# Optimization experiments

Measured on AMD Instinct MI355X. Metric: run time of the kernel, lower is better.

The kernel has to match this reference:

```python
import jax, jax.numpy as jnp
import numpy as np

NEG_SLOPE = 0.2
EPS = 1e-12


def setup_inputs() -> dict:
    key = jax.random.key(0)
    k1, k2, k3, k4, k5 = jax.random.split(key, 5)
    N, E, IN, OUT = 100000, 1600000, 256, 64
    x = jax.random.normal(k1, (N, IN), dtype=jnp.float32)
    edge_index = jax.random.randint(k2, (2, E), 0, N, dtype=jnp.int64)
    # GATConv (heads=1) parameters: lin weight, att_src, att_dst, bias
    W = jax.random.normal(k3, (IN, OUT), dtype=jnp.float32) * (1.0 / np.sqrt(IN))
    att_src = jax.random.normal(k4, (OUT,), dtype=jnp.float32) * (1.0 / np.sqrt(OUT))
    att_dst = jax.random.normal(k5, (OUT,), dtype=jnp.float32) * (1.0 / np.sqrt(OUT))
    bias = jnp.zeros((OUT,), dtype=jnp.float32)
    return {"x": x, "edge_index": edge_index, "W": W,
            "att_src": att_src, "att_dst": att_dst, "bias": bias}


def reference(x, edge_index, W, att_src, att_dst, bias):
    N = x.shape[0]
    # PyG GATConv default add_self_loops=True
    loops = jnp.arange(N, dtype=edge_index.dtype)
    src = jnp.concatenate([edge_index[0], loops])  # source j of edge (j -> i)
    dst = jnp.concatenate([edge_index[1], loops])  # target i (softmax segment)

    h = x @ W                                      # [N, out]
    a_src = h @ att_src                            # [N] per-node source score
    a_dst = h @ att_dst                            # [N] per-node target score

    e = jax.nn.leaky_relu(a_src[src] + a_dst[dst], NEG_SLOPE)  # [E+N]
    # segment softmax over incoming edges of each destination node
    e_max = jax.ops.segment_max(e, dst, num_segments=N)
    e = jnp.exp(e - e_max[dst])
    denom = jax.ops.segment_sum(e, dst, num_segments=N)
    alpha = e / denom[dst]                         # [E+N]

    # scatter-aggregate: out[i] = sum_j alpha_ij * h[j]
    out = jax.ops.segment_sum(alpha[:, None] * h[src], dst, num_segments=N)
    out = out + bias

    # dropout (p=0.3) in eval mode is identity; then F.normalize (row-wise L2)
    nrm = jnp.sqrt(jnp.sum(out * out, axis=-1, keepdims=True))
    return out / jnp.maximum(nrm, EPS)
```

## Files before the change

kernel.cpp:

```cpp
#include <hip/hip_runtime.h>
#include <hip/hip_bf16.h>
#include <math.h>

#define NEG_SLOPE 0.2f
#define EPS_NRM 1e-12f
#define K_IN 256
#define C_OUT 64
#define BK 32
#define ROWS_PB 128

__global__ __launch_bounds__(256) void gemm_att(
    const float* __restrict__ x, const float* __restrict__ W,
    const float* __restrict__ att_s, const float* __restrict__ att_d,
    __hip_bfloat16* __restrict__ h, float* __restrict__ a_src_arr,
    float* __restrict__ a_dst_arr, int N)
{
    __shared__ float xt[BK][ROWS_PB];
    __shared__ float wt[BK][C_OUT];

    int t  = threadIdx.x;
    int tx = t & 15;
    int ty = t >> 4;
    int row0 = blockIdx.x * ROWS_PB;

    int sr  = t >> 1;
    int skh = (t & 1) * 16;
    int srow = row0 + sr; if (srow >= N) srow = N - 1;
    const float* xsp = x + (size_t)srow * K_IN + skh;

    float acc[8][4];
#pragma unroll
    for (int r = 0; r < 8; ++r)
#pragma unroll
        for (int c = 0; c < 4; ++c) acc[r][c] = 0.f;

    for (int k0 = 0; k0 < K_IN; k0 += BK) {
        float4 xa = *(const float4*)(xsp + k0);
        float4 xb = *(const float4*)(xsp + k0 + 4);
        float4 xc = *(const float4*)(xsp + k0 + 8);
        float4 xd = *(const float4*)(xsp + k0 + 12);
        float4 wv4a = *(const float4*)(W + (size_t)k0 * C_OUT + t * 4);
        float4 wv4b = *(const float4*)(W + (size_t)(k0 + 16) * C_OUT + t * 4);
        __syncthreads();
        xt[skh +  0][sr] = xa.x; xt[skh +  1][sr] = xa.y;
        xt[skh +  2][sr] = xa.z; xt[skh +  3][sr] = xa.w;
        xt[skh +  4][sr] = xb.x; xt[skh +  5][sr] = xb.y;
        xt[skh +  6][sr] = xb.z; xt[skh +  7][sr] = xb.w;
        xt[skh +  8][sr] = xc.x; xt[skh +  9][sr] = xc.y;
        xt[skh + 10][sr] = xc.z; xt[skh + 11][sr] = xc.w;
        xt[skh + 12][sr] = xd.x; xt[skh + 13][sr] = xd.y;
        xt[skh + 14][sr] = xd.z; xt[skh + 15][sr] = xd.w;
        *(float4*)(&wt[ 0][0] + t * 4) = wv4a;
        *(float4*)(&wt[16][0] + t * 4) = wv4b;
        __syncthreads();

#pragma unroll
        for (int k = 0; k < BK; ++k) {
            float xv[8];
            *(float4*)&xv[0] = *(const float4*)&xt[k][ty * 8];
            *(float4*)&xv[4] = *(const float4*)&xt[k][ty * 8 + 4];
            float4 wv = *(const float4*)&wt[k][tx * 4];
#pragma unroll
            for (int r = 0; r < 8; ++r) {
                acc[r][0] += xv[r] * wv.x;
                acc[r][1] += xv[r] * wv.y;
                acc[r][2] += xv[r] * wv.z;
                acc[r][3] += xv[r] * wv.w;
            }
        }
    }

    float4 avl = *(const float4*)(att_s + tx * 4);
    float4 dvl = *(const float4*)(att_d + tx * 4);
#pragma unroll
    for (int r = 0; r < 8; ++r) {
        int row = row0 + ty * 8 + r;
        if (row >= N) continue;
        float ps = acc[r][0] * avl.x + acc[r][1] * avl.y +
                   acc[r][2] * avl.z + acc[r][3] * avl.w;
        float pd = acc[r][0] * dvl.x + acc[r][1] * dvl.y +
                   acc[r][2] * dvl.z + acc[r][3] * dvl.w;
#pragma unroll
        for (int d = 1; d < 16; d <<= 1) {
            ps += __shfl_xor(ps, d, 64);
            pd += __shfl_xor(pd, d, 64);
        }
        if (tx == 0) { a_src_arr[row] = ps; a_dst_arr[row] = pd; }
        __hip_bfloat16 hb[4];
#pragma unroll
        for (int c = 0; c < 4; ++c) hb[c] = __float2bfloat16(acc[r][c]);
        *(ushort2*)(h + (size_t)row * C_OUT + tx * 4) =
            make_ushort2(*(unsigned short*)&hb[0], *(unsigned short*)&hb[1]);
        *(ushort2*)(h + (size_t)row * C_OUT + tx * 4 + 2) =
            make_ushort2(*(unsigned short*)&hb[2], *(unsigned short*)&hb[3]);
    }
}

__global__ __launch_bounds__(256) void count_dst(
    const int* __restrict__ dst, int* __restrict__ cnt, int E)
{
    int i = blockIdx.x * blockDim.x + threadIdx.x;
    if (i < E) atomicAdd(&cnt[dst[i]], 1);
}

__global__ __launch_bounds__(256) void scan_p1(
    const int* __restrict__ cnt, int* __restrict__ partials, int n)
{
    int b = blockIdx.x, t = threadIdx.x;
    int base = b * 1024;
    int s = 0;
#pragma unroll
    for (int j = 0; j < 4; ++j) {
        int i = base + t * 4 + j;
        if (i < n) s += cnt[i] + 1;
    }
    for (int d = 1; d < 64; d <<= 1) s += __shfl_xor(s, d, 64);
    __shared__ int wsum[4];
    int lane = t & 63, wid = t >> 6;
    if (lane == 0) wsum[wid] = s;
    __syncthreads();
    if (t == 0) partials[b] = wsum[0] + wsum[1] + wsum[2] + wsum[3];
}

__global__ __launch_bounds__(256) void scan_p2(int* partials, int nb)
{
    __shared__ int buf[256];
    int t = threadIdx.x;
    int v = (t < nb) ? partials[t] : 0;
    buf[t] = v;
    __syncthreads();
    for (int d = 1; d < 256; d <<= 1) {
        int w = (t >= d) ? buf[t - d] : 0;
        __syncthreads();
        buf[t] += w;
        __syncthreads();
    }
    if (t < nb) partials[t] = buf[t] - v;
}

__global__ __launch_bounds__(256) void scan_p3(
    const int* __restrict__ cnt, const int* __restrict__ partials,
    int* __restrict__ offsets, int n)
{
    int b = blockIdx.x, t = threadIdx.x;
    int base = b * 1024;
    int v[4];
    int s = 0;
#pragma unroll
    for (int j = 0; j < 4; ++j) {
        int i = base + t * 4 + j;
        v[j] = (i < n) ? cnt[i] + 1 : 0;
        s += v[j];
    }
    int lane = t & 63, wid = t >> 6;
    int incl = s;
    for (int d = 1; d < 64; d <<= 1) {
        int w = __shfl_up(incl, d, 64);
        if (lane >= d) incl += w;
    }
    __shared__ int wsum[4];
    __shared__ int wbase[4];
    if (lane == 63) wsum[wid] = incl;
    __syncthreads();
    if (t == 0) {
        int r = 0;
        for (int i = 0; i < 4; ++i) { wbase[i] = r; r += wsum[i]; }
    }
    __syncthreads();
    int run = partials[b] + wbase[wid] + (incl - s);
#pragma unroll
    for (int j = 0; j < 4; ++j) {
        int i = base + t * 4 + j;
        if (i < n) {
            offsets[i] = run;
            run += v[j];
            if (i == n - 1) offsets[n] = run;
        }
    }
}

__global__ __launch_bounds__(256) void scatter_edges(
    const int* __restrict__ srcA, const int* __restrict__ dstA,
    const int* __restrict__ offsets, int* __restrict__ cursor,
    const float* __restrict__ a_src, const float* __restrict__ a_dst,
    int2* __restrict__ csr, int E, int N)
{
    int i = blockIdx.x * blockDim.x + threadIdx.x;
    if (i >= E + N) return;
    int s, d;
    if (i < E) { s = srcA[i]; d = dstA[i]; }
    else       { s = d = i - E; }
    float e = a_src[s] + a_dst[d];
    e = fmaxf(e, NEG_SLOPE * e);
    float w = __expf(e);
    int pos = offsets[d] + atomicAdd(&cursor[d], 1);
    int2 ent; ent.x = s; ent.y = __float_as_int(w);
    csr[pos] = ent;
}

__global__ __launch_bounds__(256) void gat_pull(
    const int* __restrict__ offsets, const int2* __restrict__ csr,
    const unsigned short* __restrict__ h, const float* __restrict__ bias,
    float* __restrict__ out, int N)
{
    int gw   = (blockIdx.x * blockDim.x + threadIdx.x) >> 6;
    int lane = threadIdx.x & 63;
    int half = lane >> 5;
    int hl   = lane & 31;
    int node = gw * 2 + half;
    bool valid = node < N;
    int nv = valid ? node : 0;

    int beg = offsets[nv];
    int n   = valid ? (offsets[nv + 1] - beg) : 0;
    const int2* ce = csr + beg;

    float2 bl = *(const float2*)(bias + 2 * hl);

    int2 c0 = ce[0];
    int2 c1 = ce[(n > 1) ? 1 : 0];
    unsigned u0 = *(const unsigned*)(h + (size_t)c0.x * C_OUT + 2 * hl);
    unsigned u1 = *(const unsigned*)(h + (size_t)c1.x * C_OUT + 2 * hl);

    float a00 = 0.f, a01 = 0.f, a10 = 0.f, a11 = 0.f, den = 0.f;
    for (int p = 0; p < n; p += 2) {
        int2 m0 = ce[(p + 2 < n) ? p + 2 : 0];
        int2 m1 = ce[(p + 3 < n) ? p + 3 : 0];
        unsigned v0 = *(const unsigned*)(h + (size_t)m0.x * C_OUT + 2 * hl);
        unsigned v1 = *(const unsigned*)(h + (size_t)m1.x * C_OUT + 2 * hl);

        float w0 = __int_as_float(c0.y);
        float w1 = (p + 1 < n) ? __int_as_float(c1.y) : 0.f;
        float h00 = __uint_as_float(u0 << 16);
        float h01 = __uint_as_float(u0 & 0xffff0000u);
        float h10 = __uint_as_float(u1 << 16);
        float h11 = __uint_as_float(u1 & 0xffff0000u);
        den += w0 + w1;
        a00 += w0 * h00; a01 += w0 * h01;
        a10 += w1 * h10; a11 += w1 * h11;

        c0 = m0; c1 = m1; u0 = v0; u1 = v1;
    }

    float o0 = (a00 + a10) / den + bl.x;
    float o1 = (a01 + a11) / den + bl.y;

    float sq = o0 * o0 + o1 * o1;
#pragma unroll
    for (int d = 1; d < 32; d <<= 1) sq += __shfl_xor(sq, d, 64);
    float nrm = fmaxf(sqrtf(sq), EPS_NRM);

    if (valid)
        *(float2*)(out + (size_t)node * C_OUT + 2 * hl) =
            make_float2(o0 / nrm, o1 / nrm);
}

extern "C" void kernel_launch(void* const* d_in, const int* in_sizes, int n_in,
                              void* d_out, int out_size, void* d_ws, size_t ws_size,
                              hipStream_t stream)
{
    const float* x     = (const float*)d_in[0];
    const int*   ei    = (const int*)d_in[1];
    const float* W     = (const float*)d_in[2];
    const float* att_s = (const float*)d_in[3];
    const float* att_d = (const float*)d_in[4];
    const float* bias  = (const float*)d_in[5];
    float*       out   = (float*)d_out;

    const int OUT = in_sizes[3];
    const int IN  = in_sizes[2] / OUT;
    const int N   = in_sizes[0] / IN;
    const int E   = in_sizes[1] / 2;

    char* w = (char*)d_ws;
    auto alloc = [&](size_t bytes) -> void* {
        void* p = (void*)w;
        w += (bytes + 255) & ~(size_t)255;
        return p;
    };
    __hip_bfloat16* h = (__hip_bfloat16*)alloc((size_t)N * C_OUT * 2);
    float* a_src  = (float*)alloc((size_t)N * 4);
    float* a_dst  = (float*)alloc((size_t)N * 4);
    int*   cnt    = (int*)alloc((size_t)N * 2 * 4);
    int*   offs   = (int*)alloc((size_t)(N + 1) * 4);
    int*   parts  = (int*)alloc(1024 * 4);
    int2*  csr    = (int2*)alloc((size_t)(E + N) * 8);
    int*   cursor = cnt + N;

    hipMemsetAsync(cnt, 0, (size_t)N * 2 * 4, stream);

    gemm_att<<<(N + ROWS_PB - 1) / ROWS_PB, 256, 0, stream>>>(
        x, W, att_s, att_d, h, a_src, a_dst, N);

    count_dst<<<(E + 255) / 256, 256, 0, stream>>>(ei + E, cnt, E);

    int NB = (N + 1023) / 1024;
    scan_p1<<<NB, 256, 0, stream>>>(cnt, parts, N);
    scan_p2<<<1, 256, 0, stream>>>(parts, NB);
    scan_p3<<<NB, 256, 0, stream>>>(cnt, parts, offs, N);

    scatter_edges<<<(E + N + 255) / 256, 256, 0, stream>>>(
        ei, ei + E, offs, cursor, a_src, a_dst, csr, E, N);

    gat_pull<<<(N + 7) / 8, 256, 0, stream>>>(offs, csr,
        (const unsigned short*)h, bias, out, N);
}
```

Before: 403.4 us.

## Handle self-loops in pull kernel, pack CSR stores, and widen per-lane feature loads

Self-loop edges are no longer written into the CSR. Each node's self term is computed directly in the pull kernel from a_src/a_dst and its own h row, which shrinks the scan counts and the scatter work. The CSR write is now a single 64-bit atomicExch of (src, weight), likely to force one 8-byte transaction. The pull kernel maps 16 lanes per node with 8-byte bf16 loads and float4 stores, putting 4 nodes in each wavefront and replacing divides with reciprocals. The atomicExch may cost more than a plain store, and nodes with no incoming edges now read a dummy entry at csr[0].

```diff
diff --git a/kernel.cpp b/kernel.cpp
--- a/kernel.cpp
+++ b/kernel.cpp
@@ -112,7 +112,7 @@
 #pragma unroll
     for (int j = 0; j < 4; ++j) {
         int i = base + t * 4 + j;
-        if (i < n) s += cnt[i] + 1;
+        if (i < n) s += cnt[i];
     }
     for (int d = 1; d < 64; d <<= 1) s += __shfl_xor(s, d, 64);
     __shared__ int wsum[4];
@@ -149,7 +149,7 @@
 #pragma unroll
     for (int j = 0; j < 4; ++j) {
         int i = base + t * 4 + j;
-        v[j] = (i < n) ? cnt[i] + 1 : 0;
+        v[j] = (i < n) ? cnt[i] : 0;
         s += v[j];
     }
     int lane = t & 63, wid = t >> 6;
@@ -183,76 +183,98 @@
     const int* __restrict__ srcA, const int* __restrict__ dstA,
     const int* __restrict__ offsets, int* __restrict__ cursor,
     const float* __restrict__ a_src, const float* __restrict__ a_dst,
-    int2* __restrict__ csr, int E, int N)
+    unsigned long long* __restrict__ csr, int E)
 {
     int i = blockIdx.x * blockDim.x + threadIdx.x;
-    if (i >= E + N) return;
-    int s, d;
-    if (i < E) { s = srcA[i]; d = dstA[i]; }
-    else       { s = d = i - E; }
+    if (i >= E) return;
+    int s = srcA[i], d = dstA[i];
     float e = a_src[s] + a_dst[d];
     e = fmaxf(e, NEG_SLOPE * e);
     float w = __expf(e);
     int pos = offsets[d] + atomicAdd(&cursor[d], 1);
-    int2 ent; ent.x = s; ent.y = __float_as_int(w);
-    csr[pos] = ent;
+    unsigned long long packed =
+        (unsigned long long)(unsigned)s |
+        ((unsigned long long)__float_as_uint(w) << 32);
+    atomicExch(&csr[pos], packed);
 }
 
 __global__ __launch_bounds__(256) void gat_pull(
     const int* __restrict__ offsets, const int2* __restrict__ csr,
-    const unsigned short* __restrict__ h, const float* __restrict__ bias,
+    const unsigned short* __restrict__ h, const float* __restrict__ a_src,
+    const float* __restrict__ a_dst, const float* __restrict__ bias,
     float* __restrict__ out, int N)
 {
     int gw   = (blockIdx.x * blockDim.x + threadIdx.x) >> 6;
     int lane = threadIdx.x & 63;
-    int half = lane >> 5;
-    int hl   = lane & 31;
-    int node = gw * 2 + half;
+    int grp  = lane >> 4;
+    int gl   = lane & 15;
+    int node = gw * 4 + grp;
     bool valid = node < N;
     int nv = valid ? node : 0;
 
     int beg = offsets[nv];
     int n   = valid ? (offsets[nv + 1] - beg) : 0;
-    const int2* ce = csr + beg;
-
-    float2 bl = *(const float2*)(bias + 2 * hl);
+    const int2* ce = csr + (n ? beg : 0);
+
+    float asv = a_src[nv], adv = a_dst[nv];
+    float es = asv + adv; es = fmaxf(es, NEG_SLOPE * es);
+    float ws = __expf(es);
+    unsigned long long hu = *(const unsigned long long*)
+        (h + (size_t)nv * C_OUT + 4 * gl);
+    unsigned hl = (unsigned)hu, hh = (unsigned)(hu >> 32);
+    float acc0 = ws * __uint_as_float(hl << 16);
+    float acc1 = ws * __uint_as_float(hl & 0xffff0000u);
+    float acc2 = ws * __uint_as_float(hh << 16);
+    float acc3 = ws * __uint_as_float(hh & 0xffff0000u);
+    float den = ws;
 
     int2 c0 = ce[0];
     int2 c1 = ce[(n > 1) ? 1 : 0];
-    unsigned u0 = *(const unsigned*)(h + (size_t)c0.x * C_OUT + 2 * hl);
-    unsigned u1 = *(const unsigned*)(h + (size_t)c1.x * C_OUT + 2 * hl);
-
-    float a00 = 0.f, a01 = 0.f, a10 = 0.f, a11 = 0.f, den = 0.f;
+    unsigned long long u0 = *(const unsigned long long*)
+        (h + (size_t)c0.x * C_OUT + 4 * gl);
+    unsigned long long u1 = *(const unsigned long long*)
+        (h + (size_t)c1.x * C_OUT + 4 * gl);
+
     for (int p = 0; p < n; p += 2) {
         int2 m0 = ce[(p + 2 < n) ? p + 2 : 0];
         int2 m1 = ce[(p + 3 < n) ? p + 3 : 0];
-        unsigned v0 = *(const unsigned*)(h + (size_t)m0.x * C_OUT + 2 * hl);
-        unsigned v1 = *(const unsigned*)(h + (size_t)m1.x * C_OUT + 2 * hl);
+        unsigned long long v0 = *(const unsigned long long*)
+            (h + (size_t)m0.x * C_OUT + 4 * gl);
+        unsigned long long v1 = *(const unsigned long long*)
+            (h + (size_t)m1.x * C_OUT + 4 * gl);
 
         float w0 = __int_as_float(c0.y);
         float w1 = (p + 1 < n) ? __int_as_float(c1.y) : 0.f;
-        float h00 = __uint_as_float(u0 << 16);
-        float h01 = __uint_as_float(u0 & 0xffff0000u);
-        float h10 = __uint_as_float(u1 << 16);
-        float h11 = __uint_as_float(u1 & 0xffff0000u);
-        den += w0 + w1;
-        a00 += w0 * h00; a01 += w0 * h01;
-        a10 += w1 * h10; a11 += w1 * h11;
+        unsigned l0 = (unsigned)u0, h0 = (unsigned)(u0 >> 32);
+        unsigned l1 = (unsigned)u1, h1 = (unsigned)(u1 >> 32);
+        den  += w0 + w1;
+        acc0 += w0 * __uint_as_float(l0 << 16)
+              + w1 * __uint_as_float(l1 << 16);
+        acc1 += w0 * __uint_as_float(l0 & 0xffff0000u)
+              + w1 * __uint_as_float(l1 & 0xffff0000u);
+        acc2 += w0 * __uint_as_float(h0 << 16)
+              + w1 * __uint_as_float(h1 << 16);
+        acc3 += w0 * __uint_as_float(h0 & 0xffff0000u)
+              + w1 * __uint_as_float(h1 & 0xffff0000u);
 
         c0 = m0; c1 = m1; u0 = v0; u1 = v1;
     }
 
-    float o0 = (a00 + a10) / den + bl.x;
-    float o1 = (a01 + a11) / den + bl.y;
-
-    float sq = o0 * o0 + o1 * o1;
-#pragma unroll
-    for (int d = 1; d < 32; d <<= 1) sq += __shfl_xor(sq, d, 64);
-    float nrm = fmaxf(sqrtf(sq), EPS_NRM);
+    float4 bl = *(const float4*)(bias + 4 * gl);
+    float rd = 1.f / den;
+    float o0 = acc0 * rd + bl.x;
+    float o1 = acc1 * rd + bl.y;
+    float o2 = acc2 * rd + bl.z;
+    float o3 = acc3 * rd + bl.w;
+
+    float sq = o0 * o0 + o1 * o1 + o2 * o2 + o3 * o3;
+#pragma unroll
+    for (int d = 1; d < 16; d <<= 1) sq += __shfl_xor(sq, d, 64);
+    float rn = 1.f / fmaxf(sqrtf(sq), EPS_NRM);
 
     if (valid)
-        *(float2*)(out + (size_t)node * C_OUT + 2 * hl) =
-            make_float2(o0 / nrm, o1 / nrm);
+        *(float4*)(out + (size_t)node * C_OUT + 4 * gl) =
+            make_float4(o0 * rn, o1 * rn, o2 * rn, o3 * rn);
 }
 
 extern "C" void kernel_launch(void* const* d_in, const int* in_sizes, int n_in,
@@ -284,7 +306,7 @@
     int*   cnt    = (int*)alloc((size_t)N * 2 * 4);
     int*   offs   = (int*)alloc((size_t)(N + 1) * 4);
     int*   parts  = (int*)alloc(1024 * 4);
-    int2*  csr    = (int2*)alloc((size_t)(E + N) * 8);
+    unsigned long long* csr = (unsigned long long*)alloc((size_t)E * 8);
     int*   cursor = cnt + N;
 
     hipMemsetAsync(cnt, 0, (size_t)N * 2 * 4, stream);
@@ -299,9 +321,9 @@
     scan_p2<<<1, 256, 0, stream>>>(parts, NB);
     scan_p3<<<NB, 256, 0, stream>>>(cnt, parts, offs, N);
 
-    scatter_edges<<<(E + N + 255) / 256, 256, 0, stream>>>(
-        ei, ei + E, offs, cursor, a_src, a_dst, csr, E, N);
-
-    gat_pull<<<(N + 7) / 8, 256, 0, stream>>>(offs, csr,
-        (const unsigned short*)h, bias, out, N);
-}
+    scatter_edges<<<(E + 255) / 256, 256, 0, stream>>>(
+        ei, ei + E, offs, cursor, a_src, a_dst, csr, E);
+
+    gat_pull<<<(N + 15) / 16, 256, 0, stream>>>(offs, (const int2*)csr,
+        (const unsigned short*)h, a_src, a_dst, bias, out, N);
+}
```

New measurement: 433.3 us. +7.4%, slower.
